# Kernel tuning notes

Hardware: AMD Instinct MI355X
Metric: run time of the kernel (lower is better)

The kernel has to match this reference:

```python
import math
import jax, jax.numpy as jnp
import numpy as np

B, S, HID = 2, 2048, 1024
NH, HD = 16, 64            # num heads, head dim (HID = NH*HD)
NB, MAXD = 32, 128         # relative attention buckets / max distance
Q_SCALING = 1.0


def setup_inputs() -> dict:
    key = jax.random.key(0)
    ks = jax.random.split(key, 6)
    return {
        "hidden_states": jax.random.normal(ks[0], (B, S, HID), dtype=jnp.float32),
        "w_qkv": jax.random.normal(ks[1], (HID, 3 * HID), dtype=jnp.float32) * 0.02,
        "b_qkv": jax.random.normal(ks[2], (3 * HID,), dtype=jnp.float32) * 0.02,
        "w_dense": jax.random.normal(ks[3], (HID, HID), dtype=jnp.float32) * 0.02,
        "b_dense": jax.random.normal(ks[4], (HID,), dtype=jnp.float32) * 0.02,
        "rel_attn_table": jax.random.normal(ks[5], (NH, NB), dtype=jnp.float32) * 0.02,
    }


def _relative_position_bucket(q_len, k_len, num_buckets, max_distance):
    # Bidirectional T5-style buckets, matching compute_relative_bias.
    ctx = jnp.arange(q_len, dtype=jnp.int32)[:, None]
    mem = jnp.arange(k_len, dtype=jnp.int32)[None, :]
    rel = mem - ctx                                     # [Q, K]
    nb = num_buckets // 2
    buckets = jnp.where(rel > 0, nb, 0)
    rel = jnp.abs(rel)
    max_exact = nb // 2
    is_small = rel < max_exact
    # log path (clamp to >=1 to avoid log(0); masked by is_small anyway)
    tmp = jnp.log(jnp.maximum(rel, 1).astype(jnp.float32) / max_exact)
    large = tmp / math.log(max_distance / max_exact) * (nb - max_exact)
    large = max_exact + large.astype(jnp.int32)
    large = jnp.minimum(large, nb - 1)
    return buckets + jnp.where(is_small, rel, large)    # [Q, K]


def reference(hidden_states, w_qkv, b_qkv, w_dense, b_dense, rel_attn_table):
    b, s, _ = hidden_states.shape
    qkv = hidden_states @ w_qkv + b_qkv                 # [B, S, 3*HID]
    q, k, v = jnp.split(qkv, 3, axis=-1)
    q = q.reshape(b, s, NH, HD)
    k = k.reshape(b, s, NH, HD)
    v = v.reshape(b, s, NH, HD)

    norm = Q_SCALING * math.sqrt(HD)
    scores = jnp.einsum("bqhd,bkhd->bhqk", q, k) / norm  # [B, H, S, S]

    buckets = _relative_position_bucket(s, s, NB, MAXD)  # [Q, K] int32
    bias = rel_attn_table[:, buckets]                    # [H, Q, K]
    scores = scores + bias[None]

    probs = jax.nn.softmax(scores, axis=-1)
    ctx = jnp.einsum("bhqk,bkhd->bqhd", probs, v).reshape(b, s, HID)
    return ctx @ w_dense + b_dense
```

## Files before the change

kernel.cpp:

```cpp
#include <hip/hip_runtime.h>
#include <hip/hip_bf16.h>
#include <math.h>

#define S_ 2048

typedef __attribute__((ext_vector_type(8))) short bf16x8;
typedef __attribute__((ext_vector_type(4))) float f32x4;
typedef __attribute__((ext_vector_type(8))) unsigned short u16x8;
typedef __attribute__((ext_vector_type(4))) unsigned short u16x4;

__device__ inline unsigned short f2bf(float f) {
  union { float f; unsigned u; } x; x.f = f;
  unsigned r = x.u + 0x7fff + ((x.u >> 16) & 1);
  return (unsigned short)(r >> 16);
}

__device__ __forceinline__ float exp2_raw(float x) {
  float r;
  asm("v_exp_f32 %0, %1" : "=v"(r) : "v"(x));
  return r;
}

__device__ __forceinline__ void gll16(const unsigned short* g, unsigned short* l) {
  __builtin_amdgcn_global_load_lds(
      (const __attribute__((address_space(1))) unsigned int*)g,
      (__attribute__((address_space(3))) unsigned int*)l, 16, 0, 0);
}

__device__ __forceinline__ void transpose_tile(
    const float* __restrict__ in, unsigned short* __restrict__ out,
    int K, int N, int bx, int by, int tid, unsigned short (*tile)[72]) {
  const int k0 = by * 64, n0 = bx * 64;
  const int rr = tid >> 4, cc = (tid & 15) * 4;
#pragma unroll
  for (int p = 0; p < 4; ++p) {
    int k = rr + p * 16;
    float4 v = *(const float4*)&in[(size_t)(k0 + k) * N + n0 + cc];
    tile[k][cc + 0] = f2bf(v.x);
    tile[k][cc + 1] = f2bf(v.y);
    tile[k][cc + 2] = f2bf(v.z);
    tile[k][cc + 3] = f2bf(v.w);
  }
  __syncthreads();
#pragma unroll
  for (int p = 0; p < 4; ++p) {
    int n = rr + p * 16;
    u16x4 o;
    o[0] = tile[cc + 0][n];
    o[1] = tile[cc + 1][n];
    o[2] = tile[cc + 2][n];
    o[3] = tile[cc + 3][n];
    *(u16x4*)&out[(size_t)(n0 + n) * K + k0 + cc] = o;
  }
}

__global__ __launch_bounds__(256) void prologue_kernel(
    const float* __restrict__ hs, unsigned short* __restrict__ hsb,
    const float* __restrict__ w_qkv, unsigned short* __restrict__ wqT,
    const float* __restrict__ w_dense, unsigned short* __restrict__ wdT,
    const float* __restrict__ table, float* __restrict__ biasTab) {
  __shared__ unsigned short tile[64][72];
  const int blk = blockIdx.x;
  const int tid = threadIdx.x;
  if (blk < 2048) {
    int i = blk * 256 + tid;
    float4 a = ((const float4*)hs)[i * 2];
    float4 b = ((const float4*)hs)[i * 2 + 1];
    u16x8 o;
    o[0] = f2bf(a.x); o[1] = f2bf(a.y); o[2] = f2bf(a.z); o[3] = f2bf(a.w);
    o[4] = f2bf(b.x); o[5] = f2bf(b.y); o[6] = f2bf(b.z); o[7] = f2bf(b.w);
    *(u16x8*)&hsb[(size_t)i * 8] = o;
  } else if (blk < 2816) {
    int t = blk - 2048;
    transpose_tile(w_qkv, wqT, 1024, 3072, t % 48, t / 48, tid, tile);
  } else if (blk < 3072) {
    int t = blk - 2816;
    transpose_tile(w_dense, wdT, 1024, 1024, t % 16, t / 16, tid, tile);
  } else {
    int idx = (blk - 3072) * 256 + tid;
    int h = idx >> 12;
    int r = idx & 4095;
    int rel = r - 2047;
    int bucket = rel > 0 ? 16 : 0;
    int ar = rel < 0 ? -rel : rel;
    if (ar < 8) {
      bucket += ar;
    } else {
      float tmp = logf((float)ar / 8.0f);
      float lf = tmp / 2.7725887222397811f * 8.0f;
      int large = 8 + (int)lf;
      bucket += (large < 15 ? large : 15);
    }
    biasTab[idx] = table[h * 32 + bucket] * 1.44269504088896f;
  }
}

template <bool BF16OUT>
__global__ __launch_bounds__(256) void gemm_mfma_kernel(
    const unsigned short* __restrict__ A, const unsigned short* __restrict__ Bt,
    const float* __restrict__ bias, void* __restrict__ Cout,
    int M, int N, int K) {
  __shared__ __align__(16) unsigned short As[128 * 64];
  __shared__ __align__(16) unsigned short Bs[128 * 64];
  const int tid = threadIdx.x;
  const int wave = tid >> 6, lane = tid & 63;
  const int lg = lane >> 4, lr = lane & 15;
  const int nbx = gridDim.x;
  const int flat = blockIdx.y * nbx + blockIdx.x;
  const int cpx = (nbx * gridDim.y) >> 3;
  const int swzid = (flat & 7) * cpx + (flat >> 3);
  const int m0 = (swzid / nbx) * 128, n0 = (swzid % nbx) * 128;
  const int wm = (wave & 1) * 64, wn = (wave >> 1) * 64;

  f32x4 acc[4][4] = {};

  const int rbase = tid >> 3;
  const int lsw = ((tid & 7) ^ (rbase & 7)) * 8;
  const unsigned short* aP[4];
  const unsigned short* bP[4];
  unsigned short* ldsA[4];
  unsigned short* ldsB[4];
#pragma unroll
  for (int g = 0; g < 4; ++g) {
    aP[g] = A + (size_t)(m0 + g * 32 + rbase) * K + lsw;
    bP[g] = Bt + (size_t)(n0 + g * 32 + rbase) * K + lsw;
    ldsA[g] = &As[g * 2048 + (tid & ~63) * 8];
    ldsB[g] = &Bs[g * 2048 + (tid & ~63) * 8];
  }

  for (int kt = 0; kt < K; kt += 64) {
    __syncthreads();
#pragma unroll
    for (int g = 0; g < 4; ++g) {
      gll16(aP[g] + kt, ldsA[g]);
      gll16(bP[g] + kt, ldsB[g]);
    }
    __syncthreads();
#pragma unroll
    for (int kh = 0; kh < 2; ++kh) {
      bf16x8 af[4], bfr[4];
#pragma unroll
      for (int t = 0; t < 4; ++t) {
        const int slot = ((kh * 4 + lg) ^ (lr & 7)) * 8;
        af[t]  = *(const bf16x8*)&As[(wm + t * 16 + lr) * 64 + slot];
        bfr[t] = *(const bf16x8*)&Bs[(wn + t * 16 + lr) * 64 + slot];
      }
#pragma unroll
      for (int i = 0; i < 4; ++i)
#pragma unroll
        for (int j = 0; j < 4; ++j)
          acc[i][j] = __builtin_amdgcn_mfma_f32_16x16x32_bf16(
              af[i], bfr[j], acc[i][j], 0, 0, 0);
    }
  }

  float bv[4];
#pragma unroll
  for (int j = 0; j < 4; ++j) bv[j] = bias[n0 + wn + j * 16 + lr];

  if constexpr (BF16OUT) {
    __syncthreads();
    unsigned short* rp = &As[wave * 1024];
#pragma unroll
    for (int i = 0; i < 4; ++i) {
#pragma unroll
      for (int j = 0; j < 4; ++j) {
        const int cw = ((j + lg) & 3) * 16 + lr;
#pragma unroll
        for (int r = 0; r < 4; ++r)
          rp[(lg * 4 + r) * 64 + cw] = f2bf(acc[i][j][r] + bv[j]);
      }
#pragma unroll
      for (int pass = 0; pass < 2; ++pass) {
        const int row = pass * 8 + (lane >> 3);
        const int cread = ((((lane & 7) >> 1) + (row >> 2)) & 3) * 16 +
                          (lane & 1) * 8;
        u16x8 v = *(const u16x8*)&rp[row * 64 + cread];
        *(u16x8*)&((unsigned short*)Cout)[
            (size_t)(m0 + wm + i * 16 + row) * N + n0 + wn + (lane & 7) * 8] = v;
      }
    }
  } else {
#pragma unroll
    for (int i = 0; i < 4; ++i)
#pragma unroll
      for (int j = 0; j < 4; ++j)
#pragma unroll
        for (int r = 0; r < 4; ++r) {
          int row = m0 + wm + i * 16 + lg * 4 + r;
          int col = n0 + wn + j * 16 + lr;
          ((float*)Cout)[(size_t)row * N + col] = acc[i][j][r] + bv[j];
        }
  }
}

template <bool BF16OUT>
__global__ __launch_bounds__(256) void gemm_mfma64_kernel(
    const unsigned short* __restrict__ A, const unsigned short* __restrict__ Bt,
    const float* __restrict__ bias, void* __restrict__ Cout,
    int M, int N, int K) {
  __shared__ __align__(16) unsigned short As[64 * 64];
  __shared__ __align__(16) unsigned short Bs[128 * 64];
  const int tid = threadIdx.x;
  const int wave = tid >> 6, lane = tid & 63;
  const int lg = lane >> 4, lr = lane & 15;
  const int nbx = gridDim.x;
  const int flat = blockIdx.y * nbx + blockIdx.x;
  const int cpx = (nbx * gridDim.y) >> 3;
  const int swzid = (flat & 7) * cpx + (flat >> 3);
  const int m0 = (swzid / nbx) * 64, n0 = (swzid % nbx) * 128;
  const int wm = (wave & 1) * 32, wn = (wave >> 1) * 64;

  f32x4 acc[2][4] = {};

  const int rbase = tid >> 3;
  const int lsw = ((tid & 7) ^ (rbase & 7)) * 8;
  const unsigned short* aP[2];
  const unsigned short* bP[4];
  unsigned short* ldsA[2];
  unsigned short* ldsB[4];
#pragma unroll
  for (int g = 0; g < 2; ++g) {
    aP[g] = A + (size_t)(m0 + g * 32 + rbase) * K + lsw;
    ldsA[g] = &As[g * 2048 + (tid & ~63) * 8];
  }
#pragma unroll
  for (int g = 0; g < 4; ++g) {
    bP[g] = Bt + (size_t)(n0 + g * 32 + rbase) * K + lsw;
    ldsB[g] = &Bs[g * 2048 + (tid & ~63) * 8];
  }

  for (int kt = 0; kt < K; kt += 64) {
    __syncthreads();
#pragma unroll
    for (int g = 0; g < 2; ++g) gll16(aP[g] + kt, ldsA[g]);
#pragma unroll
    for (int g = 0; g < 4; ++g) gll16(bP[g] + kt, ldsB[g]);
    __syncthreads();
#pragma unroll
    for (int kh = 0; kh < 2; ++kh) {
      bf16x8 af[2], bfr[4];
      const int slotb = ((kh * 4 + lg) ^ (lr & 7)) * 8;
#pragma unroll
      for (int t = 0; t < 2; ++t)
        af[t] = *(const bf16x8*)&As[(wm + t * 16 + lr) * 64 + slotb];
#pragma unroll
      for (int t = 0; t < 4; ++t)
        bfr[t] = *(const bf16x8*)&Bs[(wn + t * 16 + lr) * 64 + slotb];
#pragma unroll
      for (int i = 0; i < 2; ++i)
#pragma unroll
        for (int j = 0; j < 4; ++j)
          acc[i][j] = __builtin_amdgcn_mfma_f32_16x16x32_bf16(
              af[i], bfr[j], acc[i][j], 0, 0, 0);
    }
  }

  float bv[4];
#pragma unroll
  for (int j = 0; j < 4; ++j) bv[j] = bias[n0 + wn + j * 16 + lr];
#pragma unroll
  for (int i = 0; i < 2; ++i) {
#pragma unroll
    for (int j = 0; j < 4; ++j) {
#pragma unroll
      for (int r = 0; r < 4; ++r) {
        int row = m0 + wm + i * 16 + lg * 4 + r;
        int col = n0 + wn + j * 16 + lr;
        float val = acc[i][j][r] + bv[j];
        if constexpr (BF16OUT)
          ((unsigned short*)Cout)[(size_t)row * N + col] = f2bf(val);
        else
          ((float*)Cout)[(size_t)row * N + col] = val;
      }
    }
  }
}

__global__ __launch_bounds__(256) void vperm_kernel(
    const unsigned short* __restrict__ qkvb, unsigned short* __restrict__ vP) {
  const int t = blockIdx.x, h = blockIdx.y, bb = blockIdx.z;
  __shared__ unsigned short tile[64][72];
  const int tid = threadIdx.x;
  {
    int k = tid >> 2, c = (tid & 3) * 16;
    const unsigned short* src =
        qkvb + (size_t)(bb * S_ + t * 64 + k) * 3072 + 2048 + h * 64 + c;
    *(bf16x8*)&tile[k][c] = *(const bf16x8*)src;
    *(bf16x8*)&tile[k][c + 8] = *(const bf16x8*)(src + 8);
  }
  __syncthreads();
  const int d = tid >> 2, m0 = (tid & 3) * 16;
  unsigned short* dst =
      vP + ((size_t)((bb * 16 + h) * 64 + d)) * S_ + t * 64 + m0;
#pragma unroll
  for (int half = 0; half < 2; ++half) {
    u16x8 o;
#pragma unroll
    for (int j = 0; j < 8; ++j) {
      int m = m0 + half * 8 + j;
      int phys_s = m >> 3, e = m & 7;
      int s = phys_s ^ (d & 7);
      int w = s >> 2, lg = s & 3;
      int kw = w * 32 + (e >> 2) * 16 + lg * 4 + (e & 3);
      o[j] = tile[kw][d];
    }
    *(u16x8*)(dst + half * 8) = o;
  }
}

__global__ __launch_bounds__(512) void attn_mfma6_kernel(
    const unsigned short* __restrict__ qkvb, const unsigned short* __restrict__ vP,
    const float* __restrict__ biasTab, unsigned short* __restrict__ ctxb) {
  const int wg0 = blockIdx.x;
  const int wg = (wg0 & 7) * 64 + (wg0 >> 3);
  const int qt = wg & 15;
  const int h  = (wg >> 4) & 15;
  const int bb = wg >> 8;

  const int tid = threadIdx.x;
  const int wave = tid >> 6;
  const int lane = tid & 63;
  const int lg = lane >> 4;
  const int lr = lane & 15;

  __shared__ __align__(16) unsigned short Klds[2][4096];
  __shared__ __align__(16) unsigned short Vlds[2][4096];
  __shared__ float biasW[2][192];

  const int q0 = qt * 128;
  const int qw = q0 + wave * 16;
  const float SCL = 0.125f * 1.44269504088896f;
  const float THR = 11.5415603f;

  bf16x8 qf[2];
#pragma unroll
  for (int kh = 0; kh < 2; ++kh)
    qf[kh] = *(const bf16x8*)(qkvb +
        (size_t)(bb * S_ + qw + lr) * 3072 + h * 64 + kh * 32 + lg * 8);

  float mrun = -1e30f;
  float lpart = 0.f;
  f32x4 ov[4] = {};

  const int kk = tid >> 3, kpb = tid & 7;
  const unsigned short* kptr = qkvb + (size_t)(bb * S_ + kk) * 3072 + 1024 +
                               h * 64 + (kpb ^ (kk & 7)) * 8;
  const unsigned short* vptr = vP + ((size_t)((bb * 16 + h) * 64 + (tid >> 3))) * S_ +
                               (tid & 7) * 8;
  const float* btabH = biasTab + h * 4096 + 2047;

  auto nonuni = [&](int tt) {
    int rl = tt * 64 - q0;
    return !((rl - 127 >= 91) || (rl + 63 <= -91));
  };

  gll16(kptr, &Klds[0][(tid & ~63) * 8]);
  gll16(vptr, &Vlds[0][(tid & ~63) * 8]);
  if (nonuni(0) && tid < 192) biasW[0][tid] = btabH[-q0 - 127 + tid];

  for (int t = 0; t < 32; ++t) {
    const int cur = t & 1;
    __syncthreads();

    if (t < 31) {
      const size_t kadv = (size_t)(t + 1) * 64 * 3072;
      gll16(kptr + kadv, &Klds[cur ^ 1][(tid & ~63) * 8]);
      gll16(vptr + (t + 1) * 64, &Vlds[cur ^ 1][(tid & ~63) * 8]);
      if (nonuni(t + 1) && tid < 192)
        biasW[cur ^ 1][tid] = btabH[(t + 1) * 64 - q0 - 127 + tid];
    }

    f32x4 sc[4] = {};
    __builtin_amdgcn_s_setprio(1);
#pragma unroll
    for (int kt = 0; kt < 4; ++kt) {
      const unsigned short* kr = &Klds[cur][(kt * 16 + lr) * 64];
      bf16x8 kf0 = *(const bf16x8*)(kr + ((lg)     ^ (lr & 7)) * 8);
      bf16x8 kf1 = *(const bf16x8*)(kr + ((4 + lg) ^ (lr & 7)) * 8);
      sc[kt] = __builtin_amdgcn_mfma_f32_16x16x32_bf16(kf0, qf[0], sc[kt], 0, 0, 0);
      sc[kt] = __builtin_amdgcn_mfma_f32_16x16x32_bf16(kf1, qf[1], sc[kt], 0, 0, 0);
    }
    __builtin_amdgcn_s_setprio(0);

    bf16x8 vfr[2][4];
#pragma unroll
    for (int kh = 0; kh < 2; ++kh)
#pragma unroll
      for (int db = 0; db < 4; ++db)
        vfr[kh][db] = *(const bf16x8*)&Vlds[cur][
            (db * 16 + lr) * 64 + ((4 * kh + lg) ^ (lr & 7)) * 8];

    float pp[4][4];
    if (nonuni(t)) {
      const int bidx = 127 + lg * 4 - wave * 16 - lr;
#pragma unroll
      for (int kt = 0; kt < 4; ++kt)
#pragma unroll
        for (int r = 0; r < 4; ++r)
          pp[kt][r] = sc[kt][r] * SCL + biasW[cur][bidx + kt * 16 + r];
    } else {
      const float cb = btabH[t * 64 - q0];
#pragma unroll
      for (int kt = 0; kt < 4; ++kt)
#pragma unroll
        for (int r = 0; r < 4; ++r)
          pp[kt][r] = sc[kt][r] * SCL + cb;
    }

    float mx[8];
#pragma unroll
    for (int i = 0; i < 8; ++i)
      mx[i] = fmaxf(pp[i >> 1][(i & 1) * 2], pp[i >> 1][(i & 1) * 2 + 1]);
    float m01 = fmaxf(mx[0], mx[1]), m23 = fmaxf(mx[2], mx[3]);
    float m45 = fmaxf(mx[4], mx[5]), m67 = fmaxf(mx[6], mx[7]);
    float tm = fmaxf(fmaxf(m01, m23), fmaxf(m45, m67));

    if (!__all(tm <= mrun + THR)) {
      tm = fmaxf(tm, __shfl_xor(tm, 16));
      tm = fmaxf(tm, __shfl_xor(tm, 32));
      float mn = fmaxf(mrun, tm);
      float sfv = exp2_raw(mrun - mn);
      mrun = mn;
      lpart *= sfv;
#pragma unroll
      for (int r = 0; r < 4; ++r) {
        float sq = __shfl(sfv, (lane & 48) | (lg * 4 + r));
#pragma unroll
        for (int db = 0; db < 4; ++db) ov[db][r] *= sq;
      }
    }

#pragma unroll
    for (int kt = 0; kt < 4; ++kt)
#pragma unroll
      for (int r = 0; r < 4; ++r)
        pp[kt][r] = exp2_raw(pp[kt][r] - mrun);
    float s8[8];
#pragma unroll
    for (int i = 0; i < 8; ++i)
      s8[i] = pp[i >> 1][(i & 1) * 2] + pp[i >> 1][(i & 1) * 2 + 1];
    float s01 = s8[0] + s8[1], s23 = s8[2] + s8[3];
    float s45 = s8[4] + s8[5], s67 = s8[6] + s8[7];
    lpart += (s01 + s23) + (s45 + s67);

    union { bf16x8 v; unsigned u[4]; } pk[2];
#pragma unroll
    for (int kh = 0; kh < 2; ++kh) {
      asm("v_cvt_pk_bf16_f32 %0, %1, %2"
          : "=v"(pk[kh].u[0]) : "v"(pp[2 * kh][0]), "v"(pp[2 * kh][1]));
      asm("v_cvt_pk_bf16_f32 %0, %1, %2"
          : "=v"(pk[kh].u[1]) : "v"(pp[2 * kh][2]), "v"(pp[2 * kh][3]));
      asm("v_cvt_pk_bf16_f32 %0, %1, %2"
          : "=v"(pk[kh].u[2]) : "v"(pp[2 * kh + 1][0]), "v"(pp[2 * kh + 1][1]));
      asm("v_cvt_pk_bf16_f32 %0, %1, %2"
          : "=v"(pk[kh].u[3]) : "v"(pp[2 * kh + 1][2]), "v"(pp[2 * kh + 1][3]));
    }

    __builtin_amdgcn_s_setprio(1);
#pragma unroll
    for (int kh = 0; kh < 2; ++kh)
#pragma unroll
      for (int db = 0; db < 4; ++db)
        ov[db] = __builtin_amdgcn_mfma_f32_16x16x32_bf16(
            pk[kh].v, vfr[kh][db], ov[db], 0, 0, 0);
    __builtin_amdgcn_s_setprio(0);
  }

  float lsum = lpart;
  lsum += __shfl_xor(lsum, 16);
  lsum += __shfl_xor(lsum, 32);
  float invl = 1.0f / lsum;
#pragma unroll
  for (int r = 0; r < 4; ++r) {
    float iv = __shfl(invl, (lane & 48) | (lg * 4 + r));
    size_t row = (size_t)(bb * S_ + qw + lg * 4 + r);
#pragma unroll
    for (int db = 0; db < 4; ++db)
      ctxb[row * 1024 + h * 64 + db * 16 + lr] = f2bf(ov[db][r] * iv);
  }
}

extern "C" void kernel_launch(void* const* d_in, const int* in_sizes, int n_in,
                              void* d_out, int out_size, void* d_ws, size_t ws_size,
                              hipStream_t stream) {
  const float* hs      = (const float*)d_in[0];
  const float* w_qkv   = (const float*)d_in[1];
  const float* b_qkv   = (const float*)d_in[2];
  const float* w_dense = (const float*)d_in[3];
  const float* b_dense = (const float*)d_in[4];
  const float* rtab    = (const float*)d_in[5];
  float* out = (float*)d_out;

  char* ws = (char*)d_ws;
  unsigned short* qkvb = (unsigned short*)ws;
  unsigned short* ctxb = (unsigned short*)(ws + (((size_t)24) << 20));
  unsigned short* hsb  = (unsigned short*)(ws + (((size_t)32) << 20));
  unsigned short* wqT  = (unsigned short*)(ws + (((size_t)40) << 20));
  unsigned short* wdT  = (unsigned short*)(ws + (((size_t)46) << 20));
  unsigned short* vP   = (unsigned short*)(ws + (((size_t)48) << 20));
  float* biasTab       = (float*)(ws + (((size_t)56) << 20));

  hipLaunchKernelGGL(prologue_kernel, dim3(3328), dim3(256), 0, stream,
                     hs, hsb, w_qkv, wqT, w_dense, wdT, rtab, biasTab);
  hipLaunchKernelGGL((gemm_mfma_kernel<true>), dim3(24, 32), dim3(256), 0, stream,
                     hsb, wqT, b_qkv, (void*)qkvb, 4096, 3072, 1024);
  hipLaunchKernelGGL(vperm_kernel, dim3(32, 16, 2), dim3(256), 0, stream,
                     qkvb, vP);
  hipLaunchKernelGGL(attn_mfma6_kernel, dim3(512), dim3(512), 0, stream,
                     qkvb, vP, biasTab, ctxb);
  hipLaunchKernelGGL((gemm_mfma64_kernel<false>), dim3(8, 64), dim3(256), 0, stream,
                     ctxb, wdT, b_dense, (void*)out, 4096, 1024, 1024);
}
```

Baseline: 129.0 us.

## Fuse V permutation into QKV GEMM epilogue and drop vperm kernel

The QKV GEMM epilogue now writes the V columns (n0 >= 2048) directly into the permuted, swizzled vP layout through an LDS staging buffer, instead of writing them to qkvb. The separate vperm kernel, which re-read V from global memory and transposed it, is removed. This saves one launch plus a read and write of the V tensor. In exchange the GEMM epilogue becomes more complex, and the new layout mapping has to match what the attention kernel expects.

```diff
diff --git a/kernel.cpp b/kernel.cpp
--- a/kernel.cpp
+++ b/kernel.cpp
@@ -99,7 +99,7 @@
 __global__ __launch_bounds__(256) void gemm_mfma_kernel(
     const unsigned short* __restrict__ A, const unsigned short* __restrict__ Bt,
     const float* __restrict__ bias, void* __restrict__ Cout,
-    int M, int N, int K) {
+    unsigned short* __restrict__ vP, int M, int N, int K) {
   __shared__ __align__(16) unsigned short As[128 * 64];
   __shared__ __align__(16) unsigned short Bs[128 * 64];
   const int tid = threadIdx.x;
@@ -160,24 +160,55 @@
 
   if constexpr (BF16OUT) {
     __syncthreads();
-    unsigned short* rp = &As[wave * 1024];
-#pragma unroll
-    for (int i = 0; i < 4; ++i) {
-#pragma unroll
-      for (int j = 0; j < 4; ++j) {
-        const int cw = ((j + lg) & 3) * 16 + lr;
-#pragma unroll
-        for (int r = 0; r < 4; ++r)
-          rp[(lg * 4 + r) * 64 + cw] = f2bf(acc[i][j][r] + bv[j]);
+    if (n0 < 2048) {
+      unsigned short* rp = &As[wave * 1024];
+#pragma unroll
+      for (int i = 0; i < 4; ++i) {
+#pragma unroll
+        for (int j = 0; j < 4; ++j) {
+          const int cw = ((j + lg) & 3) * 16 + lr;
+#pragma unroll
+          for (int r = 0; r < 4; ++r)
+            rp[(lg * 4 + r) * 64 + cw] = f2bf(acc[i][j][r] + bv[j]);
+        }
+#pragma unroll
+        for (int pass = 0; pass < 2; ++pass) {
+          const int row = pass * 8 + (lane >> 3);
+          const int cread = ((((lane & 7) >> 1) + (row >> 2)) & 3) * 16 +
+                            (lane & 1) * 8;
+          u16x8 v = *(const u16x8*)&rp[row * 64 + cread];
+          *(u16x8*)&((unsigned short*)Cout)[
+              (size_t)(m0 + wm + i * 16 + row) * N + n0 + wn + (lane & 7) * 8] = v;
+        }
       }
-#pragma unroll
-      for (int pass = 0; pass < 2; ++pass) {
-        const int row = pass * 8 + (lane >> 3);
-        const int cread = ((((lane & 7) >> 1) + (row >> 2)) & 3) * 16 +
-                          (lane & 1) * 8;
-        u16x8 v = *(const u16x8*)&rp[row * 64 + cread];
-        *(u16x8*)&((unsigned short*)Cout)[
-            (size_t)(m0 + wm + i * 16 + row) * N + n0 + wn + (lane & 7) * 8] = v;
+    } else {
+      unsigned short* R = (wave < 2) ? &As[(wave & 1) * 4096]
+                                     : &Bs[(wave & 1) * 4096];
+#pragma unroll
+      for (int i = 0; i < 4; ++i) {
+        const int lsv = (i >> 1) * 4 + lg;
+        const int ebase = (i & 1) * 4;
+#pragma unroll
+        for (int j = 0; j < 4; ++j) {
+          const int d = j * 16 + lr;
+          const int ps = lsv ^ (d & 7);
+          u16x4 o;
+#pragma unroll
+          for (int r = 0; r < 4; ++r) o[r] = f2bf(acc[i][j][r] + bv[j]);
+          *(u16x4*)&R[d * 64 + ps * 8 + ebase] = o;
+        }
+      }
+      const int krow0 = m0 + wm;
+      const int bbv = krow0 >> 11;
+      const int sbase = krow0 & 2047;
+      const int h = ((n0 - 2048) >> 6) + (wave >> 1);
+#pragma unroll
+      for (int it = 0; it < 8; ++it) {
+        const int d = it * 8 + (lane >> 3);
+        const int c = lane & 7;
+        u16x8 v = *(const u16x8*)&R[d * 64 + c * 8];
+        *(u16x8*)&vP[((size_t)((bbv * 16 + h) * 64 + d)) * 2048 +
+                     sbase + c * 8] = v;
       }
     }
   } else {
@@ -277,38 +308,6 @@
   }
 }
 
-__global__ __launch_bounds__(256) void vperm_kernel(
-    const unsigned short* __restrict__ qkvb, unsigned short* __restrict__ vP) {
-  const int t = blockIdx.x, h = blockIdx.y, bb = blockIdx.z;
-  __shared__ unsigned short tile[64][72];
-  const int tid = threadIdx.x;
-  {
-    int k = tid >> 2, c = (tid & 3) * 16;
-    const unsigned short* src =
-        qkvb + (size_t)(bb * S_ + t * 64 + k) * 3072 + 2048 + h * 64 + c;
-    *(bf16x8*)&tile[k][c] = *(const bf16x8*)src;
-    *(bf16x8*)&tile[k][c + 8] = *(const bf16x8*)(src + 8);
-  }
-  __syncthreads();
-  const int d = tid >> 2, m0 = (tid & 3) * 16;
-  unsigned short* dst =
-      vP + ((size_t)((bb * 16 + h) * 64 + d)) * S_ + t * 64 + m0;
-#pragma unroll
-  for (int half = 0; half < 2; ++half) {
-    u16x8 o;
-#pragma unroll
-    for (int j = 0; j < 8; ++j) {
-      int m = m0 + half * 8 + j;
-      int phys_s = m >> 3, e = m & 7;
-      int s = phys_s ^ (d & 7);
-      int w = s >> 2, lg = s & 3;
-      int kw = w * 32 + (e >> 2) * 16 + lg * 4 + (e & 3);
-      o[j] = tile[kw][d];
-    }
-    *(u16x8*)(dst + half * 8) = o;
-  }
-}
-
 __global__ __launch_bounds__(512) void attn_mfma6_kernel(
     const unsigned short* __restrict__ qkvb, const unsigned short* __restrict__ vP,
     const float* __restrict__ biasTab, unsigned short* __restrict__ ctxb) {
@@ -504,9 +503,7 @@
   hipLaunchKernelGGL(prologue_kernel, dim3(3328), dim3(256), 0, stream,
                      hs, hsb, w_qkv, wqT, w_dense, wdT, rtab, biasTab);
   hipLaunchKernelGGL((gemm_mfma_kernel<true>), dim3(24, 32), dim3(256), 0, stream,
-                     hsb, wqT, b_qkv, (void*)qkvb, 4096, 3072, 1024);
-  hipLaunchKernelGGL(vperm_kernel, dim3(32, 16, 2), dim3(256), 0, stream,
-                     qkvb, vP);
+                     hsb, wqT, b_qkv, (void*)qkvb, vP, 4096, 3072, 1024);
   hipLaunchKernelGGL(attn_mfma6_kernel, dim3(512), dim3(512), 0, stream,
                      qkvb, vP, biasTab, ctxb);
   hipLaunchKernelGGL((gemm_mfma64_kernel<false>), dim3(8, 64), dim3(256), 0, stream,
```

Result: no change. 127.3 us (median of 2 runs) (-1.3%).
